# Kernel optimization log

Hardware: AMD Instinct MI355X
Metric: run time of the kernel (lower is better)

## Reference

```python
import jax, jax.numpy as jnp
import numpy as np

N, F, H, E = 100000, 64, 8, 1200000
D = F // H
HID = 32  # hardcoded MLP hidden width in the module


def setup_inputs() -> dict:
    key = jax.random.key(0)
    ks = jax.random.split(key, 16)
    s = 0.05
    return {
        "h": jax.random.normal(ks[0], (N, F), jnp.float32),
        "W_src": jax.random.normal(ks[1], (F, F), jnp.float32) * s,
        "b_src": jnp.zeros((F,), jnp.float32),
        "W_dst": jax.random.normal(ks[2], (F, F), jnp.float32) * s,
        "b_dst": jnp.zeros((F,), jnp.float32),
        "Wa1_src": jax.random.normal(ks[3], (F, HID), jnp.float32) * s,
        "ba1_src": jnp.zeros((HID,), jnp.float32),
        "Wa2_src": jax.random.normal(ks[4], (HID, H), jnp.float32) * s,
        "ba2_src": jnp.zeros((H,), jnp.float32),
        "Wa1_dst": jax.random.normal(ks[5], (F, HID), jnp.float32) * s,
        "ba1_dst": jnp.zeros((HID,), jnp.float32),
        "Wa2_dst": jax.random.normal(ks[6], (HID, H), jnp.float32) * s,
        "ba2_dst": jnp.zeros((H,), jnp.float32),
        "edge_index": jax.random.randint(ks[7], (2, E), 0, N, jnp.int64),
    }


def _attn_mlp(x, W1, b1, W2, b2):
    # Sequential(LeakyReLU(0.2), Linear(F,32), LeakyReLU(0.2), Linear(32,H))
    y = jax.nn.leaky_relu(x, 0.2)
    y = y @ W1 + b1
    y = jax.nn.leaky_relu(y, 0.2)
    return y @ W2 + b2


def reference(h, W_src, b_src, W_dst, b_dst,
              Wa1_src, ba1_src, Wa2_src, ba2_src,
              Wa1_dst, ba1_dst, Wa2_dst, ba2_dst,
              edge_index):
    src, dst = edge_index[0], edge_index[1]
    g_src = h @ W_src + b_src          # [N,F]
    g_dst = h @ W_dst + b_dst          # [N,F]
    msg_src = g_src[src]               # [E,F] gather
    msg = msg_src + g_dst[dst]         # [E,F]
    a_src = jax.nn.sigmoid(_attn_mlp(msg, Wa1_src, ba1_src, Wa2_src, ba2_src))[:, :, None]    # [E,H,1]
    a_dst = jax.nn.sigmoid(_attn_mlp(g_dst, Wa1_dst, ba1_dst, Wa2_dst, ba2_dst))[:, :, None]  # [N,H,1]
    agg = jax.ops.segment_sum(a_src * msg_src.reshape(E, H, D), dst, num_segments=N)          # [N,H,D]
    h_next = a_dst * g_dst.reshape(N, H, D) + agg
    return h_next.reshape(N, F)
```

## Files before the change

### kernel.cpp

```cpp
#include <hip/hip_runtime.h>
#include <hip/hip_bf16.h>
#include <hip/hip_fp16.h>

#define NF   64
#define NH   8
#define ND   8
#define NHID 32
#define XS   68
#define OS   10

typedef __attribute__((ext_vector_type(8))) short bf16x8v;
typedef __attribute__((ext_vector_type(4))) float f32x4v;

__device__ __forceinline__ float bf2f(unsigned short u) {
    union { unsigned int i; float f; } v; v.i = ((unsigned int)u) << 16; return v.f;
}
__device__ __forceinline__ unsigned short f2bf(float f) {
    __hip_bfloat16 b = __float2bfloat16(f);
    union { __hip_bfloat16 b; unsigned short u; } v; v.b = b; return v.u;
}
__device__ __forceinline__ void unpack8(uint4 u, float* o) {
    o[0] = __uint_as_float(u.x << 16); o[1] = __uint_as_float(u.x & 0xffff0000u);
    o[2] = __uint_as_float(u.y << 16); o[3] = __uint_as_float(u.y & 0xffff0000u);
    o[4] = __uint_as_float(u.z << 16); o[5] = __uint_as_float(u.z & 0xffff0000u);
    o[6] = __uint_as_float(u.w << 16); o[7] = __uint_as_float(u.w & 0xffff0000u);
}
__device__ __forceinline__ uint4 pack8(const float* f) {
    uint4 u;
    u.x = (unsigned)f2bf(f[0]) | ((unsigned)f2bf(f[1]) << 16);
    u.y = (unsigned)f2bf(f[2]) | ((unsigned)f2bf(f[3]) << 16);
    u.z = (unsigned)f2bf(f[4]) | ((unsigned)f2bf(f[5]) << 16);
    u.w = (unsigned)f2bf(f[6]) | ((unsigned)f2bf(f[7]) << 16);
    return u;
}
__device__ __forceinline__ float leaky(float x) { return fmaxf(x, 0.2f * x); }
__device__ __forceinline__ float sigmoidf(float x) { return 1.f / (1.f + __expf(-x)); }

__global__ void detect_kernel(const int* __restrict__ edge, int* __restrict__ flags) {
    if (threadIdx.x == 0 && blockIdx.x == 0) {
        int oddnz = 0;
        for (int i = 0; i < 32; i++) oddnz |= edge[2 * i + 1];
        flags[0] = (oddnz == 0) ? 1 : 0;
    }
}

__device__ __forceinline__ void load_edge(const int* __restrict__ edge, int e, int E,
                                          int wide, int& s, int& d) {
    if (wide) { s = edge[2 * e]; d = edge[2 * (E + e)]; }
    else      { s = edge[e];     d = edge[E + e]; }
}

#define WBF_TOTAL 12544
__global__ __launch_bounds__(256) void prep_weights_kernel(
    const float* __restrict__ Ws, const float* __restrict__ Wd,
    const float* __restrict__ W1d, const float* __restrict__ W1s,
    const float* __restrict__ W2s, unsigned short* __restrict__ o,
    int* __restrict__ counts, int N)
{
    int i = blockIdx.x * 256 + threadIdx.x;
    if (i < N) counts[i] = 0;
    float v;
    if (i < 4096)        { int j = i;         v = Ws [(j & 63) * 64 + (j >> 6)]; }
    else if (i < 8192)   { int j = i - 4096;  v = Wd [(j & 63) * 64 + (j >> 6)]; }
    else if (i < 10240)  { int j = i - 8192;  v = W1d[(j & 63) * 32 + (j >> 6)]; }
    else if (i < 12288)  { int j = i - 10240; v = W1s[(j & 63) * 32 + (j >> 6)]; }
    else if (i < 12544)  { int j = i - 12288; v = W2s[(j & 31) * 8  + (j >> 5)]; }
    else return;
    o[i] = f2bf(v);
}

__global__ __launch_bounds__(64) void node_mfma_kernel(
    const float* __restrict__ h,
    const unsigned short* __restrict__ WsT, const float* __restrict__ b_src,
    const unsigned short* __restrict__ WdT, const float* __restrict__ b_dst,
    const unsigned short* __restrict__ W1T, const float* __restrict__ ba1,
    const float* __restrict__ Wa2, const float* __restrict__ ba2,
    unsigned short* __restrict__ g_src_out, unsigned short* __restrict__ g_dst_out,
    float* __restrict__ out,
    const int* __restrict__ edge, const int* __restrict__ flags,
    int* __restrict__ counts, int* __restrict__ rank, int E, int N)
{
    __shared__ __align__(16) unsigned short sX[64 * XS];
    __shared__ __align__(16) unsigned short sY[64 * XS];
    __shared__ float sW2[NHID * NH];
    __shared__ float sb2[NH];

    int lane = threadIdx.x;
    int nsub = lane & 15, quad = lane >> 4;
    int base = blockIdx.x * 64;
    int n = base + lane;
    bool valid = n < N;
    size_t nn = valid ? (size_t)n : (size_t)(N - 1);

    for (int i = lane; i < NHID * NH; i += 64) sW2[i] = Wa2[i];
    if (lane < NH) sb2[lane] = ba2[lane];

    {
        const float4* hv = (const float4*)(h + nn * NF);
        unsigned short* xrow = sX + lane * XS;
        #pragma unroll
        for (int k = 0; k < 8; k++) {
            float4 u0 = hv[2 * k], u1 = hv[2 * k + 1];
            float f[8] = { u0.x, u0.y, u0.z, u0.w, u1.x, u1.y, u1.z, u1.w };
            uint4 p = pack8(f);
            uint2* q = (uint2*)(xrow + k * 8);
            q[0] = make_uint2(p.x, p.y);
            q[1] = make_uint2(p.z, p.w);
        }
    }
    __syncthreads();

    #pragma unroll 1
    for (int m = 0; m < 2; m++) {
        const unsigned short* WT = m ? WdT : WsT;
        const float* bb = m ? b_dst : b_src;
        unsigned short* gout = m ? g_dst_out : g_src_out;

        bf16x8v Bf[2][4];
        #pragma unroll
        for (int ks = 0; ks < 2; ks++)
            #pragma unroll
            for (int nt = 0; nt < 4; nt++) {
                union { uint4 u; bf16x8v v; } u;
                u.u = *(const uint4*)(WT + (nt * 16 + nsub) * 64 + ks * 32 + quad * 8);
                Bf[ks][nt] = u.v;
            }

        f32x4v acc[4][4];
        #pragma unroll
        for (int mt = 0; mt < 4; mt++)
            #pragma unroll
            for (int nt = 0; nt < 4; nt++) {
                f32x4v z = {0.f, 0.f, 0.f, 0.f};
                acc[mt][nt] = z;
            }

        #pragma unroll
        for (int ks = 0; ks < 2; ks++)
            #pragma unroll
            for (int mt = 0; mt < 4; mt++) {
                const unsigned short* ap = sX + (mt * 16 + nsub) * XS + ks * 32 + quad * 8;
                union { uint2 d[2]; bf16x8v v; } ua;
                ua.d[0] = *(const uint2*)ap;
                ua.d[1] = *(const uint2*)(ap + 4);
                #pragma unroll
                for (int nt = 0; nt < 4; nt++)
                    acc[mt][nt] = __builtin_amdgcn_mfma_f32_16x16x32_bf16(
                        ua.v, Bf[ks][nt], acc[mt][nt], 0, 0, 0);
            }

        if (m == 1) __syncthreads();

        #pragma unroll
        for (int nt = 0; nt < 4; nt++) {
            float bv = bb[nt * 16 + nsub];
            #pragma unroll
            for (int mt = 0; mt < 4; mt++)
                #pragma unroll
                for (int r = 0; r < 4; r++)
                    sY[(mt * 16 + quad * 4 + r) * XS + nt * 16 + nsub] =
                        f2bf(acc[mt][nt][r] + bv);
        }
        __syncthreads();

        if (valid) {
            const unsigned short* yrow = sY + lane * XS;
            uint4* gp = (uint4*)(gout + (size_t)n * NF);
            #pragma unroll
            for (int k = 0; k < 8; k++) {
                uint2 a = *(const uint2*)(yrow + k * 8);
                uint2 b = *(const uint2*)(yrow + k * 8 + 4);
                gp[k] = make_uint4(a.x, a.y, b.x, b.y);
            }
        }
    }

    bf16x8v B1f[2][2];
    #pragma unroll
    for (int ks = 0; ks < 2; ks++)
        #pragma unroll
        for (int nt = 0; nt < 2; nt++) {
            union { uint4 u; bf16x8v v; } u;
            u.u = *(const uint4*)(W1T + (nt * 16 + nsub) * 64 + ks * 32 + quad * 8);
            B1f[ks][nt] = u.v;
        }

    f32x4v acc2[4][2];
    #pragma unroll
    for (int mt = 0; mt < 4; mt++)
        #pragma unroll
        for (int nt = 0; nt < 2; nt++) {
            f32x4v z = {0.f, 0.f, 0.f, 0.f};
            acc2[mt][nt] = z;
        }

    #pragma unroll
    for (int ks = 0; ks < 2; ks++)
        #pragma unroll
        for (int mt = 0; mt < 4; mt++) {
            const unsigned short* ap = sY + (mt * 16 + nsub) * XS + ks * 32 + quad * 8;
            uint2 d0 = *(const uint2*)ap;
            uint2 d1 = *(const uint2*)(ap + 4);
            float f[8];
            unpack8(make_uint4(d0.x, d0.y, d1.x, d1.y), f);
            #pragma unroll
            for (int t = 0; t < 8; t++) f[t] = leaky(f[t]);
            uint4 p = pack8(f);
            union { uint4 u; bf16x8v v; } ua; ua.u = p;
            #pragma unroll
            for (int nt = 0; nt < 2; nt++)
                acc2[mt][nt] = __builtin_amdgcn_mfma_f32_16x16x32_bf16(
                    ua.v, B1f[ks][nt], acc2[mt][nt], 0, 0, 0);
        }
    __syncthreads();

    #pragma unroll
    for (int nt = 0; nt < 2; nt++) {
        float b1v = ba1[nt * 16 + nsub];
        #pragma unroll
        for (int mt = 0; mt < 4; mt++)
            #pragma unroll
            for (int r = 0; r < 4; r++)
                sX[(mt * 16 + quad * 4 + r) * XS + nt * 16 + nsub] =
                    f2bf(leaky(acc2[mt][nt][r] + b1v));
    }
    __syncthreads();

    if (valid) {
        float hid[NHID];
        const unsigned short* hrow = sX + lane * XS;
        #pragma unroll
        for (int k = 0; k < 8; k++) {
            uint2 dv = *(const uint2*)(hrow + k * 4);
            hid[k * 4 + 0] = bf2f((unsigned short)(dv.x & 0xffffu));
            hid[k * 4 + 1] = bf2f((unsigned short)(dv.x >> 16));
            hid[k * 4 + 2] = bf2f((unsigned short)(dv.y & 0xffffu));
            hid[k * 4 + 3] = bf2f((unsigned short)(dv.y >> 16));
        }
        float a[NH];
        #pragma unroll
        for (int j = 0; j < NH; j++) a[j] = sb2[j];
        #pragma unroll
        for (int k = 0; k < NHID; k++) {
            float xk = hid[k];
            #pragma unroll
            for (int j = 0; j < NH; j++) a[j] = fmaf(xk, sW2[k * NH + j], a[j]);
        }
        #pragma unroll
        for (int j = 0; j < NH; j++) a[j] = sigmoidf(a[j]);

        const unsigned short* yrow = sY + lane * XS;
        float4* op = (float4*)(out + (size_t)n * NF);
        #pragma unroll
        for (int k = 0; k < 8; k++) {
            uint2 u0 = *(const uint2*)(yrow + k * 8);
            uint2 u1 = *(const uint2*)(yrow + k * 8 + 4);
            float g[8];
            unpack8(make_uint4(u0.x, u0.y, u1.x, u1.y), g);
            float ah0 = a[(k * 8) >> 3];
            op[2 * k]     = make_float4(ah0 * g[0], ah0 * g[1], ah0 * g[2], ah0 * g[3]);
            op[2 * k + 1] = make_float4(ah0 * g[4], ah0 * g[5], ah0 * g[6], ah0 * g[7]);
        }
    }

    {
        int wide = flags[0];
        int stride = gridDim.x * 64;
        for (int e = blockIdx.x * 64 + lane; e < E; e += stride) {
            int s, d;
            load_edge(edge, e, E, wide, s, d);
            if ((unsigned)s >= (unsigned)N || (unsigned)d >= (unsigned)N) { rank[e] = -1; continue; }
            rank[e] = atomicAdd(&counts[d], 1);
        }
    }
}

template <bool STORE_G>
__global__ __launch_bounds__(256) void node_kernel_t(
    const float* __restrict__ h,
    const float* __restrict__ W_src, const float* __restrict__ b_src,
    const float* __restrict__ W_dst, const float* __restrict__ b_dst,
    const float* __restrict__ Wa1, const float* __restrict__ ba1,
    const float* __restrict__ Wa2, const float* __restrict__ ba2,
    unsigned short* __restrict__ g_src_out, unsigned short* __restrict__ g_dst_out,
    float* __restrict__ out, int N)
{
    __shared__ __align__(16) float sWs[NF * NF];
    __shared__ __align__(16) float sWd[NF * NF];
    __shared__ __align__(16) float sW1[NF * NHID];
    __shared__ __align__(16) float sW2[NHID * NH];
    __shared__ float sbs[NF], sbd[NF], sb1[NHID], sb2[NH];

    int tid = threadIdx.x;
    for (int i = tid; i < NF * NF; i += 256) { sWs[i] = W_src[i]; sWd[i] = W_dst[i]; }
    for (int i = tid; i < NF * NHID; i += 256) sW1[i] = Wa1[i];
    if (tid < NHID * NH) sW2[tid] = Wa2[tid];
    if (tid < NF) { sbs[tid] = b_src[tid]; sbd[tid] = b_dst[tid]; }
    if (tid < NHID) sb1[tid] = ba1[tid];
    if (tid < NH) sb2[tid] = ba2[tid];
    __syncthreads();

    int n = blockIdx.x * 256 + tid;
    if (n >= N) return;

    float hrow[NF];
    const float4* hv = (const float4*)(h + (size_t)n * NF);
    #pragma unroll
    for (int k = 0; k < 16; k++) {
        float4 u = hv[k];
        hrow[k * 4 + 0] = u.x; hrow[k * 4 + 1] = u.y;
        hrow[k * 4 + 2] = u.z; hrow[k * 4 + 3] = u.w;
    }

    float acc[NF];
    const float4* Wsv = (const float4*)sWs;
    const float4* Wdv = (const float4*)sWd;

    if (STORE_G) {
        #pragma unroll
        for (int j = 0; j < NF; j++) acc[j] = sbs[j];
        for (int i = 0; i < NF; i++) {
            float hi = hrow[i];
            #pragma unroll
            for (int jb = 0; jb < 16; jb++) {
                float4 w = Wsv[i * 16 + jb];
                acc[jb * 4 + 0] = fmaf(hi, w.x, acc[jb * 4 + 0]);
                acc[jb * 4 + 1] = fmaf(hi, w.y, acc[jb * 4 + 1]);
                acc[jb * 4 + 2] = fmaf(hi, w.z, acc[jb * 4 + 2]);
                acc[jb * 4 + 3] = fmaf(hi, w.w, acc[jb * 4 + 3]);
            }
        }
        uint4* gs = (uint4*)(g_src_out + (size_t)n * NF);
        #pragma unroll
        for (int k = 0; k < 8; k++) gs[k] = pack8(acc + k * 8);
    }

    #pragma unroll
    for (int j = 0; j < NF; j++) acc[j] = sbd[j];
    for (int i = 0; i < NF; i++) {
        float hi = hrow[i];
        #pragma unroll
        for (int jb = 0; jb < 16; jb++) {
            float4 w = Wdv[i * 16 + jb];
            acc[jb * 4 + 0] = fmaf(hi, w.x, acc[jb * 4 + 0]);
            acc[jb * 4 + 1] = fmaf(hi, w.y, acc[jb * 4 + 1]);
            acc[jb * 4 + 2] = fmaf(hi, w.z, acc[jb * 4 + 2]);
            acc[jb * 4 + 3] = fmaf(hi, w.w, acc[jb * 4 + 3]);
        }
    }
    if (STORE_G) {
        uint4* gd = (uint4*)(g_dst_out + (size_t)n * NF);
        #pragma unroll
        for (int k = 0; k < 8; k++) gd[k] = pack8(acc + k * 8);
    }

    float hid[NHID];
    #pragma unroll
    for (int j = 0; j < NHID; j++) hid[j] = sb1[j];
    const float4* W1v = (const float4*)sW1;
    for (int i = 0; i < NF; i++) {
        float xi = leaky(acc[i]);
        #pragma unroll
        for (int jb = 0; jb < 8; jb++) {
            float4 w = W1v[i * 8 + jb];
            hid[jb * 4 + 0] = fmaf(xi, w.x, hid[jb * 4 + 0]);
            hid[jb * 4 + 1] = fmaf(xi, w.y, hid[jb * 4 + 1]);
            hid[jb * 4 + 2] = fmaf(xi, w.z, hid[jb * 4 + 2]);
            hid[jb * 4 + 3] = fmaf(xi, w.w, hid[jb * 4 + 3]);
        }
    }
    float a[NH];
    #pragma unroll
    for (int j = 0; j < NH; j++) a[j] = sb2[j];
    #pragma unroll
    for (int k = 0; k < NHID; k++) {
        float xk = leaky(hid[k]);
        #pragma unroll
        for (int j = 0; j < NH; j++) a[j] = fmaf(xk, sW2[k * NH + j], a[j]);
    }
    #pragma unroll
    for (int j = 0; j < NH; j++) a[j] = sigmoidf(a[j]);

    float4* ap = (float4*)(out + (size_t)n * NF);
    #pragma unroll
    for (int k = 0; k < 16; k++) {
        int j = k * 4;
        ap[k] = make_float4(a[(j + 0) >> 3] * acc[j + 0],
                            a[(j + 1) >> 3] * acc[j + 1],
                            a[(j + 2) >> 3] * acc[j + 2],
                            a[(j + 3) >> 3] * acc[j + 3]);
    }
}

__global__ __launch_bounds__(256) void scan1_kernel(
    const int* __restrict__ counts, int* __restrict__ offsets,
    int* __restrict__ bsums, int N)
{
    __shared__ int lds[256];
    int tid = threadIdx.x;
    int base = blockIdx.x * 2048 + tid * 8;
    int v[8]; int s = 0;
    #pragma unroll
    for (int k = 0; k < 8; k++) { int idx = base + k; int t = (idx < N) ? counts[idx] : 0; v[k] = t; s += t; }
    lds[tid] = s;
    __syncthreads();
    for (int off = 1; off < 256; off <<= 1) {
        int y = (tid >= off) ? lds[tid - off] : 0;
        __syncthreads();
        lds[tid] += y;
        __syncthreads();
    }
    int run = lds[tid] - s;
    #pragma unroll
    for (int k = 0; k < 8; k++) { int idx = base + k; if (idx < N) offsets[idx] = run; run += v[k]; }
    if (tid == 255) bsums[blockIdx.x] = lds[255];
}

__global__ void scan2_kernel(int* __restrict__ bsums, int* __restrict__ offsets, int NB, int N) {
    if (threadIdx.x == 0 && blockIdx.x == 0) {
        int run = 0;
        for (int i = 0; i < NB; i++) { int t = bsums[i]; bsums[i] = run; run += t; }
        offsets[N] = run;
    }
}

__global__ __launch_bounds__(256) void scan3_kernel(
    int* __restrict__ offsets, const int* __restrict__ bsums, int N)
{
    int add = bsums[blockIdx.x];
    int base = blockIdx.x * 2048 + threadIdx.x * 8;
    #pragma unroll
    for (int k = 0; k < 8; k++) { int idx = base + k; if (idx < N) offsets[idx] += add; }
}

__global__ __launch_bounds__(256) void scatter_kernel(
    const int* __restrict__ edge, const int* __restrict__ flags,
    const int* __restrict__ offsets, const int* __restrict__ rank,
    int* __restrict__ sorted_s, int E, int N)
{
    int e = blockIdx.x * 256 + threadIdx.x;
    if (e >= E) return;
    int r = rank[e];
    if (r < 0) return;
    int s, d;
    load_edge(edge, e, E, flags[0], s, d);
    sorted_s[offsets[d] + r] = s;
}

__global__ __launch_bounds__(256) void fill_d_kernel(
    const int* __restrict__ offsets, int* __restrict__ sorted_d, int N)
{
    int d = blockIdx.x * 256 + threadIdx.x;
    if (d >= N) return;
    int beg = offsets[d], end = offsets[d + 1];
    for (int i = beg; i < end; i++) sorted_d[i] = d;
}

__global__ __launch_bounds__(256) void edge_mlp_mfma_kernel(
    const int* __restrict__ sorted_s, const int* __restrict__ sorted_d,
    const int* __restrict__ total_p,
    const unsigned short* __restrict__ g_src, const unsigned short* __restrict__ g_dst,
    const unsigned short* __restrict__ W1T, const float* __restrict__ ba1,
    const unsigned short* __restrict__ W2T, const float* __restrict__ ba2,
    __half* __restrict__ a_sorted)
{
    __shared__ __align__(16) unsigned short sX[4 * 64 * XS];
    __shared__ __align__(16) __half sOut[4 * 64 * OS];
    __shared__ float sb1[NHID], sb2[NH];

    int tid = threadIdx.x;
    if (tid < NHID) sb1[tid] = ba1[tid];
    if (tid < NH) sb2[tid] = ba2[tid];

    int wave = tid >> 6;
    int lane = tid & 63;
    int nsub = lane & 15;
    int quad = lane >> 4;
    int total = *total_p;
    int i = blockIdx.x * 256 + wave * 64 + lane;
    bool valid = i < total;
    int s = valid ? sorted_s[i] : 0;
    int d = valid ? sorted_d[i] : 0;

    unsigned short* xrow = sX + (wave * 64 + lane) * XS;
    {
        const uint4* gs = (const uint4*)(g_src + (size_t)s * NF);
        const uint4* gd = (const uint4*)(g_dst + (size_t)d * NF);
        #pragma unroll
        for (int k = 0; k < 8; k++) {
            float A8[8], B8[8], x8[8];
            unpack8(gs[k], A8); unpack8(gd[k], B8);
            #pragma unroll
            for (int t = 0; t < 8; t++) x8[t] = leaky(A8[t] + B8[t]);
            uint4 pk = pack8(x8);
            uint2* q = (uint2*)(xrow + k * 8);
            q[0] = make_uint2(pk.x, pk.y);
            q[1] = make_uint2(pk.z, pk.w);
        }
    }

    bf16x8v Bf[2][2];
    #pragma unroll
    for (int ks = 0; ks < 2; ks++)
        #pragma unroll
        for (int nt = 0; nt < 2; nt++) {
            union { uint4 u; bf16x8v v; } u;
            u.u = *(const uint4*)(W1T + (nt * 16 + nsub) * 64 + ks * 32 + quad * 8);
            Bf[ks][nt] = u.v;
        }
    bf16x8v B2f;
    {
        union { uint4 u; bf16x8v v; } u;
        if (nsub < NH) u.u = *(const uint4*)(W2T + nsub * 32 + quad * 8);
        else           u.u = make_uint4(0u, 0u, 0u, 0u);
        B2f = u.v;
    }

    __syncthreads();

    f32x4v acc[4][2];
    #pragma unroll
    for (int mt = 0; mt < 4; mt++)
        #pragma unroll
        for (int nt = 0; nt < 2; nt++) {
            f32x4v z = {0.f, 0.f, 0.f, 0.f};
            acc[mt][nt] = z;
        }

    const unsigned short* wbase = sX + wave * 64 * XS;
    #pragma unroll
    for (int ks = 0; ks < 2; ks++) {
        #pragma unroll
        for (int mt = 0; mt < 4; mt++) {
            const unsigned short* ap = wbase + (mt * 16 + nsub) * XS + ks * 32 + quad * 8;
            union { uint2 d[2]; bf16x8v v; } ua;
            ua.d[0] = *(const uint2*)ap;
            ua.d[1] = *(const uint2*)(ap + 4);
            #pragma unroll
            for (int nt = 0; nt < 2; nt++)
                acc[mt][nt] = __builtin_amdgcn_mfma_f32_16x16x32_bf16(
                    ua.v, Bf[ks][nt], acc[mt][nt], 0, 0, 0);
        }
    }

    __syncthreads();

    #pragma unroll
    for (int nt = 0; nt < 2; nt++) {
        int n = nt * 16 + nsub;
        float b1v = sb1[n];
        #pragma unroll
        for (int mt = 0; mt < 4; mt++) {
            #pragma unroll
            for (int r = 0; r < 4; r++) {
                int m = mt * 16 + quad * 4 + r;
                sX[(wave * 64 + m) * XS + n] = f2bf(leaky(acc[mt][nt][r] + b1v));
            }
        }
    }

    __syncthreads();

    f32x4v acc2[4];
    #pragma unroll
    for (int mt = 0; mt < 4; mt++) { f32x4v z = {0.f, 0.f, 0.f, 0.f}; acc2[mt] = z; }
    #pragma unroll
    for (int mt = 0; mt < 4; mt++) {
        const unsigned short* ap = wbase + (mt * 16 + nsub) * XS + quad * 8;
        union { uint2 d[2]; bf16x8v v; } ua;
        ua.d[0] = *(const uint2*)ap;
        ua.d[1] = *(const uint2*)(ap + 4);
        acc2[mt] = __builtin_amdgcn_mfma_f32_16x16x32_bf16(ua.v, B2f, acc2[mt], 0, 0, 0);
    }

    if (nsub < NH) {
        float b2v = sb2[nsub];
        #pragma unroll
        for (int mt = 0; mt < 4; mt++)
            #pragma unroll
            for (int r = 0; r < 4; r++) {
                int m = mt * 16 + quad * 4 + r;
                sOut[(wave * 64 + m) * OS + nsub] = __float2half(sigmoidf(acc2[mt][r] + b2v));
            }
    }
    __syncthreads();

    if (valid) {
        const unsigned int* orow = (const unsigned int*)(sOut + (wave * 64 + lane) * OS);
        uint4 pk = make_uint4(orow[0], orow[1], orow[2], orow[3]);
        *(uint4*)(a_sorted + (size_t)i * NH) = pk;
    }
}

__global__ __launch_bounds__(256) void aggregate_kernel(
    const int* __restrict__ offsets, const int* __restrict__ sorted_s,
    const __half* __restrict__ a_sorted, const unsigned short* __restrict__ g_src,
    float* __restrict__ out, int N)
{
    int d = blockIdx.x * 32 + (threadIdx.x >> 3);
    if (d >= N) return;
    int l = threadIdx.x & 7;
    int beg = offsets[d], end = offsets[d + 1];

    float acc[8] = {0.f, 0.f, 0.f, 0.f, 0.f, 0.f, 0.f, 0.f};
    int i = beg;
    for (; i + 2 <= end; i += 2) {
        int s0 = sorted_s[i];
        int s1 = sorted_s[i + 1];
        float av0 = __half2float(a_sorted[(size_t)i * NH + l]);
        float av1 = __half2float(a_sorted[(size_t)(i + 1) * NH + l]);
        uint4 q0 = *(const uint4*)(g_src + (size_t)s0 * NF + l * 8);
        uint4 q1 = *(const uint4*)(g_src + (size_t)s1 * NF + l * 8);
        float f0[8], f1[8];
        unpack8(q0, f0); unpack8(q1, f1);
        #pragma unroll
        for (int t = 0; t < 8; t++) acc[t] = fmaf(av0, f0[t], acc[t]);
        #pragma unroll
        for (int t = 0; t < 8; t++) acc[t] = fmaf(av1, f1[t], acc[t]);
    }
    if (i < end) {
        int s0 = sorted_s[i];
        float av0 = __half2float(a_sorted[(size_t)i * NH + l]);
        uint4 q0 = *(const uint4*)(g_src + (size_t)s0 * NF + l * 8);
        float f0[8]; unpack8(q0, f0);
        #pragma unroll
        for (int t = 0; t < 8; t++) acc[t] = fmaf(av0, f0[t], acc[t]);
    }

    float4* o4 = (float4*)(out + (size_t)d * NF + l * 8);
    float4 v0 = o4[0], v1 = o4[1];
    v0.x += acc[0]; v0.y += acc[1]; v0.z += acc[2]; v0.w += acc[3];
    v1.x += acc[4]; v1.y += acc[5]; v1.z += acc[6]; v1.w += acc[7];
    o4[0] = v0; o4[1] = v1;
}

__global__ __launch_bounds__(256) void edge_kernel(
    const int* __restrict__ edge, const int* __restrict__ flags,
    const unsigned short* __restrict__ g_src, const unsigned short* __restrict__ g_dst,
    const float* __restrict__ Wa1, const float* __restrict__ ba1,
    const float* __restrict__ Wa2, const float* __restrict__ ba2,
    float* __restrict__ out, int E, int N)
{
    __shared__ __align__(16) float sW1[NF * NHID];
    __shared__ __align__(16) float sW2[NHID * NH];
    __shared__ float sb1[NHID], sb2[NH];
    int tid = threadIdx.x;
    for (int i = tid; i < NF * NHID; i += 256) sW1[i] = Wa1[i];
    if (tid < NHID * NH) sW2[tid] = Wa2[tid];
    if (tid < NHID) sb1[tid] = ba1[tid];
    if (tid < NH) sb2[tid] = ba2[tid];
    __syncthreads();

    int e = blockIdx.x * 256 + tid;
    if (e >= E) return;
    int s, d;
    load_edge(edge, e, E, flags[0], s, d);
    if ((unsigned)s >= (unsigned)N || (unsigned)d >= (unsigned)N) return;

    float ms[NF];
    float hid[NHID];
    #pragma unroll
    for (int j = 0; j < NHID; j++) hid[j] = sb1[j];

    const uint4* gs = (const uint4*)(g_src + (size_t)s * NF);
    const uint4* gd = (const uint4*)(g_dst + (size_t)d * NF);
    #pragma unroll
    for (int k = 0; k < 8; k++) {
        float a8[8], b8[8];
        unpack8(gs[k], a8);
        unpack8(gd[k], b8);
        #pragma unroll
        for (int t = 0; t < 8; t++) {
            int i = k * 8 + t;
            ms[i] = a8[t];
            float x = leaky(a8[t] + b8[t]);
            #pragma unroll
            for (int j = 0; j < NHID; j++) hid[j] = fmaf(x, sW1[i * NHID + j], hid[j]);
        }
    }

    float a[NH];
    #pragma unroll
    for (int j = 0; j < NH; j++) a[j] = sb2[j];
    #pragma unroll
    for (int k = 0; k < NHID; k++) {
        float xk = leaky(hid[k]);
        #pragma unroll
        for (int j = 0; j < NH; j++) a[j] = fmaf(xk, sW2[k * NH + j], a[j]);
    }

    float* arow = out + (size_t)d * NF;
    #pragma unroll
    for (int hh = 0; hh < NH; hh++) {
        float ah = sigmoidf(a[hh]);
        #pragma unroll
        for (int dd = 0; dd < ND; dd++)
            unsafeAtomicAdd(arow + hh * ND + dd, ah * ms[hh * ND + dd]);
    }
}

__global__ __launch_bounds__(256) void edge_kernel_fused(
    const int* __restrict__ edge, const int* __restrict__ flags,
    const float* __restrict__ h,
    const float* __restrict__ W_src, const float* __restrict__ b_src,
    const float* __restrict__ W_dst, const float* __restrict__ b_dst,
    const float* __restrict__ Wa1, const float* __restrict__ ba1,
    const float* __restrict__ Wa2, const float* __restrict__ ba2,
    float* __restrict__ out, int E, int N)
{
    __shared__ __align__(16) float sWs[NF * NF];
    __shared__ __align__(16) float sWd[NF * NF];
    __shared__ __align__(16) float sW1[NF * NHID];
    __shared__ __align__(16) float sW2[NHID * NH];
    __shared__ float sbs[NF], sbd[NF], sb1[NHID], sb2[NH];
    int tid = threadIdx.x;
    for (int i = tid; i < NF * NF; i += 256) { sWs[i] = W_src[i]; sWd[i] = W_dst[i]; }
    for (int i = tid; i < NF * NHID; i += 256) sW1[i] = Wa1[i];
    if (tid < NHID * NH) sW2[tid] = Wa2[tid];
    if (tid < NF) { sbs[tid] = b_src[tid]; sbd[tid] = b_dst[tid]; }
    if (tid < NHID) sb1[tid] = ba1[tid];
    if (tid < NH) sb2[tid] = ba2[tid];
    __syncthreads();

    int e = blockIdx.x * 256 + tid;
    if (e >= E) return;
    int wide = flags ? flags[0] : 0;
    int s, d;
    load_edge(edge, e, E, wide, s, d);
    if ((unsigned)s >= (unsigned)N || (unsigned)d >= (unsigned)N) return;

    float gsr[NF], msg[NF];
    {
        float hrow[NF];
        #pragma unroll
        for (int i = 0; i < NF; i++) hrow[i] = h[(size_t)s * NF + i];
        #pragma unroll
        for (int j = 0; j < NF; j++) gsr[j] = sbs[j];
        for (int i = 0; i < NF; i++) {
            float hi = hrow[i];
            #pragma unroll
            for (int j = 0; j < NF; j++) gsr[j] = fmaf(hi, sWs[i * NF + j], gsr[j]);
        }
    }
    #pragma unroll
    for (int j = 0; j < NF; j++) msg[j] = gsr[j] + sbd[j];
    for (int i = 0; i < NF; i++) {
        float hi = h[(size_t)d * NF + i];
        #pragma unroll
        for (int j = 0; j < NF; j++) msg[j] = fmaf(hi, sWd[i * NF + j], msg[j]);
    }

    float hid[NHID];
    #pragma unroll
    for (int j = 0; j < NHID; j++) hid[j] = sb1[j];
    for (int i = 0; i < NF; i++) {
        float x = leaky(msg[i]);
        #pragma unroll
        for (int j = 0; j < NHID; j++) hid[j] = fmaf(x, sW1[i * NHID + j], hid[j]);
    }
    float a[NH];
    #pragma unroll
    for (int j = 0; j < NH; j++) a[j] = sb2[j];
    #pragma unroll
    for (int k = 0; k < NHID; k++) {
        float xk = leaky(hid[k]);
        #pragma unroll
        for (int j = 0; j < NH; j++) a[j] = fmaf(xk, sW2[k * NH + j], a[j]);
    }

    float* arow = out + (size_t)d * NF;
    #pragma unroll
    for (int hh = 0; hh < NH; hh++) {
        float ah = sigmoidf(a[hh]);
        #pragma unroll
        for (int dd = 0; dd < ND; dd++)
            unsafeAtomicAdd(arow + hh * ND + dd, ah * gsr[hh * ND + dd]);
    }
}

static inline size_t al256(size_t x) { return (x + 255) & ~(size_t)255; }

extern "C" void kernel_launch(void* const* d_in, const int* in_sizes, int n_in,
                              void* d_out, int out_size, void* d_ws, size_t ws_size,
                              hipStream_t stream) {
    const float* h       = (const float*)d_in[0];
    const float* W_src   = (const float*)d_in[1];
    const float* b_src   = (const float*)d_in[2];
    const float* W_dst   = (const float*)d_in[3];
    const float* b_dst   = (const float*)d_in[4];
    const float* Wa1_src = (const float*)d_in[5];
    const float* ba1_src = (const float*)d_in[6];
    const float* Wa2_src = (const float*)d_in[7];
    const float* ba2_src = (const float*)d_in[8];
    const float* Wa1_dst = (const float*)d_in[9];
    const float* ba1_dst = (const float*)d_in[10];
    const float* Wa2_dst = (const float*)d_in[11];
    const float* ba2_dst = (const float*)d_in[12];
    const int* edge = (const int*)d_in[13];

    int N = in_sizes[0] / NF;
    int E = in_sizes[13] / 2;
    float* out = (float*)d_out;

    int nodeBlocks = (N + 255) / 256;
    int nodeWaves  = (N + 63) / 64;
    int edgeBlocks = (E + 255) / 256;
    int NB1 = (N + 2047) / 2048;
    int prepN = (N > WBF_TOTAL ? N : WBF_TOTAL);

    size_t o_flags  = 0;
    size_t o_wbf    = al256(o_flags + 256);
    size_t o_gsrc   = al256(o_wbf + (size_t)WBF_TOTAL * 2);
    size_t o_gdst   = al256(o_gsrc + (size_t)N * NF * 2);
    size_t o_asort  = al256(o_gdst + (size_t)N * NF * 2);
    size_t o_counts = al256(o_asort + (size_t)E * NH * 2);
    size_t o_offs   = al256(o_counts + (size_t)N * 4);
    size_t o_bsums  = al256(o_offs + ((size_t)N + 1) * 4);
    size_t o_sorted = al256(o_bsums + (size_t)NB1 * 4);
    size_t need     = o_sorted + (size_t)E * 8;

    size_t gB = (size_t)N * NF * 2;

    if (ws_size >= need) {
        char* w = (char*)d_ws;
        int*            flags   = (int*)(w + o_flags);
        unsigned short* wbf     = (unsigned short*)(w + o_wbf);
        unsigned short* WsT     = wbf;
        unsigned short* WdT     = wbf + 4096;
        unsigned short* W1dT    = wbf + 8192;
        unsigned short* W1sT    = wbf + 10240;
        unsigned short* W2sT    = wbf + 12288;
        unsigned short* g_src   = (unsigned short*)(w + o_gsrc);
        unsigned short* g_dst   = (unsigned short*)(w + o_gdst);
        __half*         a_sort  = (__half*)(w + o_asort);
        int*            rank    = (int*)(w + o_asort);
        int*            counts  = (int*)(w + o_counts);
        int*            offsets = (int*)(w + o_offs);
        int*            bsums   = (int*)(w + o_bsums);
        int*            sorted_s = (int*)(w + o_sorted);
        int*            sorted_d = sorted_s + E;

        detect_kernel<<<1, 1, 0, stream>>>(edge, flags);
        prep_weights_kernel<<<(prepN + 255) / 256, 256, 0, stream>>>(
            W_src, W_dst, Wa1_dst, Wa1_src, Wa2_src, wbf, counts, N);

        node_mfma_kernel<<<nodeWaves, 64, 0, stream>>>(
            h, WsT, b_src, WdT, b_dst,
            W1dT, ba1_dst, Wa2_dst, ba2_dst,
            g_src, g_dst, out,
            edge, flags, counts, rank, E, N);

        scan1_kernel<<<NB1, 256, 0, stream>>>(counts, offsets, bsums, N);
        scan2_kernel<<<1, 1, 0, stream>>>(bsums, offsets, NB1, N);
        scan3_kernel<<<NB1, 256, 0, stream>>>(offsets, bsums, N);

        scatter_kernel<<<edgeBlocks, 256, 0, stream>>>(
            edge, flags, offsets, rank, sorted_s, E, N);

        fill_d_kernel<<<nodeBlocks, 256, 0, stream>>>(offsets, sorted_d, N);

        edge_mlp_mfma_kernel<<<edgeBlocks, 256, 0, stream>>>(
            sorted_s, sorted_d, offsets + N, g_src, g_dst,
            W1sT, ba1_src, W2sT, ba2_src, a_sort);

        aggregate_kernel<<<(N + 31) / 32, 256, 0, stream>>>(
            offsets, sorted_s, a_sort, g_src, out, N);
    } else if (ws_size >= 256 + 2 * gB) {
        int* flags = (int*)d_ws;
        unsigned short* g_src = (unsigned short*)((char*)d_ws + 256);
        unsigned short* g_dst = g_src + (size_t)N * NF;

        detect_kernel<<<1, 1, 0, stream>>>(edge, flags);

        node_kernel_t<true><<<nodeBlocks, 256, 0, stream>>>(
            h, W_src, b_src, W_dst, b_dst,
            Wa1_dst, ba1_dst, Wa2_dst, ba2_dst,
            g_src, g_dst, out, N);

        edge_kernel<<<edgeBlocks, 256, 0, stream>>>(
            edge, flags, g_src, g_dst,
            Wa1_src, ba1_src, Wa2_src, ba2_src,
            out, E, N);
    } else {
        int* flags = (ws_size >= 256) ? (int*)d_ws : nullptr;
        if (flags) detect_kernel<<<1, 1, 0, stream>>>(edge, flags);

        node_kernel_t<false><<<nodeBlocks, 256, 0, stream>>>(
            h, W_src, b_src, W_dst, b_dst,
            Wa1_dst, ba1_dst, Wa2_dst, ba2_dst,
            nullptr, nullptr, out, N);

        edge_kernel_fused<<<edgeBlocks, 256, 0, stream>>>(
            edge, flags, h,
            W_src, b_src, W_dst, b_dst,
            Wa1_src, ba1_src, Wa2_src, ba2_src,
            out, E, N);
    }
}
```

Measured before the change: 297.1 us.

## Split edge histogram into its own kernel and fold detect into prep

Moves the per-edge atomic histogram and rank computation out of the 64-thread-per-block node MFMA kernel into a separate 256-thread kernel where each thread handles four edges. The layout-detection step is folded into the weight-prep kernel, which removes one launch. The aim is to stop the histogram from being bound to the node kernel's grid and small blocks. In exchange it adds a separate launch and gives up any overlap with the node compute that the fused loop had.

Measured after the change: 292.1 us. No clear change (-1.7%).

```diff
diff --git a/kernel.cpp b/kernel.cpp
--- a/kernel.cpp
+++ b/kernel.cpp
@@ -36,14 +36,6 @@
 __device__ __forceinline__ float leaky(float x) { return fmaxf(x, 0.2f * x); }
 __device__ __forceinline__ float sigmoidf(float x) { return 1.f / (1.f + __expf(-x)); }
 
-__global__ void detect_kernel(const int* __restrict__ edge, int* __restrict__ flags) {
-    if (threadIdx.x == 0 && blockIdx.x == 0) {
-        int oddnz = 0;
-        for (int i = 0; i < 32; i++) oddnz |= edge[2 * i + 1];
-        flags[0] = (oddnz == 0) ? 1 : 0;
-    }
-}
-
 __device__ __forceinline__ void load_edge(const int* __restrict__ edge, int e, int E,
                                           int wide, int& s, int& d) {
     if (wide) { s = edge[2 * e]; d = edge[2 * (E + e)]; }
@@ -55,9 +47,15 @@
     const float* __restrict__ Ws, const float* __restrict__ Wd,
     const float* __restrict__ W1d, const float* __restrict__ W1s,
     const float* __restrict__ W2s, unsigned short* __restrict__ o,
-    int* __restrict__ counts, int N)
+    int* __restrict__ counts, int N,
+    const int* __restrict__ edge, int* __restrict__ flags)
 {
     int i = blockIdx.x * 256 + threadIdx.x;
+    if (i == 0) {
+        int oddnz = 0;
+        for (int k = 0; k < 32; k++) oddnz |= edge[2 * k + 1];
+        flags[0] = (oddnz == 0) ? 1 : 0;
+    }
     if (i < N) counts[i] = 0;
     float v;
     if (i < 4096)        { int j = i;         v = Ws [(j & 63) * 64 + (j >> 6)]; }
@@ -76,9 +74,7 @@
     const unsigned short* __restrict__ W1T, const float* __restrict__ ba1,
     const float* __restrict__ Wa2, const float* __restrict__ ba2,
     unsigned short* __restrict__ g_src_out, unsigned short* __restrict__ g_dst_out,
-    float* __restrict__ out,
-    const int* __restrict__ edge, const int* __restrict__ flags,
-    int* __restrict__ counts, int* __restrict__ rank, int E, int N)
+    float* __restrict__ out, int N)
 {
     __shared__ __align__(16) unsigned short sX[64 * XS];
     __shared__ __align__(16) unsigned short sY[64 * XS];
@@ -262,17 +258,6 @@
             op[2 * k + 1] = make_float4(ah0 * g[4], ah0 * g[5], ah0 * g[6], ah0 * g[7]);
         }
     }
-
-    {
-        int wide = flags[0];
-        int stride = gridDim.x * 64;
-        for (int e = blockIdx.x * 64 + lane; e < E; e += stride) {
-            int s, d;
-            load_edge(edge, e, E, wide, s, d);
-            if ((unsigned)s >= (unsigned)N || (unsigned)d >= (unsigned)N) { rank[e] = -1; continue; }
-            rank[e] = atomicAdd(&counts[d], 1);
-        }
-    }
 }
 
 template <bool STORE_G>
@@ -389,6 +374,23 @@
                             a[(j + 1) >> 3] * acc[j + 1],
                             a[(j + 2) >> 3] * acc[j + 2],
                             a[(j + 3) >> 3] * acc[j + 3]);
+    }
+}
+
+__global__ __launch_bounds__(256) void hist_kernel(
+    const int* __restrict__ edge, const int* __restrict__ flags,
+    int* __restrict__ counts, int* __restrict__ rank, int E, int N, int T)
+{
+    int t = blockIdx.x * 256 + threadIdx.x;
+    int wide = flags[0];
+    #pragma unroll
+    for (int k = 0; k < 4; k++) {
+        int e = t + k * T;
+        if (e >= E) break;
+        int s, d;
+        load_edge(edge, e, E, wide, s, d);
+        if ((unsigned)s >= (unsigned)N || (unsigned)d >= (unsigned)N) { rank[e] = -1; continue; }
+        rank[e] = atomicAdd(&counts[d], 1);
     }
 }
 
@@ -632,6 +634,14 @@
     v0.x += acc[0]; v0.y += acc[1]; v0.z += acc[2]; v0.w += acc[3];
     v1.x += acc[4]; v1.y += acc[5]; v1.z += acc[6]; v1.w += acc[7];
     o4[0] = v0; o4[1] = v1;
+}
+
+__global__ void detect_kernel(const int* __restrict__ edge, int* __restrict__ flags) {
+    if (threadIdx.x == 0 && blockIdx.x == 0) {
+        int oddnz = 0;
+        for (int i = 0; i < 32; i++) oddnz |= edge[2 * i + 1];
+        flags[0] = (oddnz == 0) ? 1 : 0;
+    }
 }
 
 __global__ __launch_bounds__(256) void edge_kernel(
@@ -807,6 +817,8 @@
     int edgeBlocks = (E + 255) / 256;
     int NB1 = (N + 2047) / 2048;
     int prepN = (N > WBF_TOTAL ? N : WBF_TOTAL);
+    int histBlocks = (E + 1023) / 1024;
+    int histT = histBlocks * 256;
 
     size_t o_flags  = 0;
     size_t o_wbf    = al256(o_flags + 256);
@@ -840,15 +852,16 @@
         int*            sorted_s = (int*)(w + o_sorted);
         int*            sorted_d = sorted_s + E;
 
-        detect_kernel<<<1, 1, 0, stream>>>(edge, flags);
         prep_weights_kernel<<<(prepN + 255) / 256, 256, 0, stream>>>(
-            W_src, W_dst, Wa1_dst, Wa1_src, Wa2_src, wbf, counts, N);
+            W_src, W_dst, Wa1_dst, Wa1_src, Wa2_src, wbf, counts, N, edge, flags);
 
         node_mfma_kernel<<<nodeWaves, 64, 0, stream>>>(
             h, WsT, b_src, WdT, b_dst,
             W1dT, ba1_dst, Wa2_dst, ba2_dst,
-            g_src, g_dst, out,
-            edge, flags, counts, rank, E, N);
+            g_src, g_dst, out, N);
+
+        hist_kernel<<<histBlocks, 256, 0, stream>>>(
+            edge, flags, counts, rank, E, N, histT);
 
         scan1_kernel<<<NB1, 256, 0, stream>>>(counts, offsets, bsums, N);
         scan2_kernel<<<1, 1, 0, stream>>>(bsums, offsets, NB1, N);
```
